# Kernel tuning notes

Measured on AMD Instinct MI355X. Metric: run time of the kernel, lower is better.

The kernel has to match this reference:

```python
import jax, jax.numpy as jnp
import numpy as np

NUM_HEADS = 16
HEAD_DIM = 64
ROPE_BASE = 160000.0


def _rope_tables(seq_len, head_dim):
    inv_freq = 1.0 / (ROPE_BASE ** (jnp.arange(0, head_dim, 2, dtype=jnp.float32) / head_dim))
    freqs = jnp.arange(seq_len, dtype=jnp.float32)[:, None] * inv_freq[None, :]  # [S, hd/2]
    return jnp.cos(freqs)[None, None], jnp.sin(freqs)[None, None]  # [1,1,S,hd/2]


def _apply_rope(x, cos, sin):
    # x: [B, nh, S, hd]; split-half rotation as in the torch module
    x1, x2 = jnp.split(x, 2, axis=-1)
    return jnp.concatenate([x1 * cos - x2 * sin, x2 * cos + x1 * sin], axis=-1)


def setup_inputs() -> dict:
    key = jax.random.key(0)
    k1, k2, k3 = jax.random.split(key, 3)
    B, S, H = 2, 2048, 1024
    hidden_states = jax.random.normal(k1, (B, S, H), dtype=jnp.float32)
    # additive causal mask: 0 for allowed, -1e9 for future positions
    causal = jnp.tril(jnp.ones((S, S), dtype=bool))
    attention_mask = jnp.where(causal, 0.0, -1e9).astype(jnp.float32)[None, None]
    Wqkv = jax.random.normal(k2, (H, 3 * H), dtype=jnp.float32) * (H ** -0.5)
    Wo = jax.random.normal(k3, (H, H), dtype=jnp.float32) * (H ** -0.5)
    return {"hidden_states": hidden_states, "attention_mask": attention_mask, "Wqkv": Wqkv, "Wo": Wo}


def reference(hidden_states, attention_mask, Wqkv, Wo):
    B, S, H = hidden_states.shape
    nh, hd = NUM_HEADS, HEAD_DIM
    scale = hd ** -0.5

    qkv = hidden_states @ Wqkv                                   # [B,S,3H]
    qkv = qkv.reshape(B, S, 3, nh, hd).transpose(2, 0, 3, 1, 4)  # [3,B,nh,S,hd]
    q, k, v = qkv[0], qkv[1], qkv[2]

    cos, sin = _rope_tables(S, hd)
    q = _apply_rope(q, cos, sin)
    k = _apply_rope(k, cos, sin)

    scores = jnp.einsum('bhqd,bhkd->bhqk', q, k) * scale + attention_mask
    attn = jax.nn.softmax(scores, axis=-1)
    out = jnp.einsum('bhqk,bhkd->bhqd', attn, v)                 # [B,nh,S,hd]
    out = out.transpose(0, 2, 1, 3).reshape(B, S, H)
    return out @ Wo
```

## Files before the change

kernel.cpp:

```cpp
#include <hip/hip_runtime.h>
#include <hip/hip_bf16.h>

typedef __bf16 bf16x8 __attribute__((ext_vector_type(8)));
typedef float f32x4 __attribute__((ext_vector_type(4)));
typedef unsigned short u16;

__device__ __forceinline__ u16 f2bf(float f) {
    union { float f; unsigned u; } x{f};
    unsigned r = x.u + 0x7fffu + ((x.u >> 16) & 1u);
    return (u16)(r >> 16);
}
__device__ __forceinline__ unsigned pk2(float a, float b) {
    union { float f; unsigned u; } x{a}, y{b};
    return ((x.u + 0x8000u) >> 16) | ((y.u + 0x8000u) & 0xffff0000u);
}
__device__ __forceinline__ float ex2(float x) { return __builtin_amdgcn_exp2f(x); }
__device__ __forceinline__ f32x4 zero4() { f32x4 z = {0.f, 0.f, 0.f, 0.f}; return z; }

typedef const __attribute__((address_space(1))) unsigned int* gp1_t;
typedef __attribute__((address_space(3))) unsigned int* lp3_t;
__device__ __forceinline__ void async16(const u16* g, u16* l) {
    __builtin_amdgcn_global_load_lds((gp1_t)g, (lp3_t)l, 16, 0, 0);
}

__global__ void __launch_bounds__(256) prep(const float* __restrict__ hs,
                                            u16* __restrict__ Xb,
                                            const float* __restrict__ Wqkv,
                                            u16* __restrict__ Wqkvt,
                                            const float* __restrict__ Wo,
                                            u16* __restrict__ Wot,
                                            float* __restrict__ cosT,
                                            float* __restrict__ sinT) {
    __shared__ float tile[32][33];
    const int blk = blockIdx.x, t = threadIdx.x;
    if (blk < 4096) {
        int i = (blk * 256 + t) * 4;
        float4 v = *(const float4*)(hs + i);
        ushort4 o;
        o.x = f2bf(v.x); o.y = f2bf(v.y); o.z = f2bf(v.z); o.w = f2bf(v.w);
        *(ushort4*)(Xb + i) = o;
    } else if (blk < 8192) {
        const float* W; u16* Wt; int N, bx, by;
        if (blk < 7168) { int bid = blk - 4096; W = Wqkv; Wt = Wqkvt; N = 3072; bx = bid % 96; by = bid / 96; }
        else            { int bid = blk - 7168; W = Wo;   Wt = Wot;   N = 1024; bx = bid % 32; by = bid / 32; }
        const int K = 1024;
        int tx = t & 31, ty = t >> 5;
        int n0 = bx * 32, k0 = by * 32;
#pragma unroll
        for (int i = 0; i < 32; i += 8)
            tile[ty + i][tx] = W[(size_t)(k0 + ty + i) * N + n0 + tx];
        __syncthreads();
#pragma unroll
        for (int i = 0; i < 32; i += 8)
            Wt[(size_t)(n0 + ty + i) * K + k0 + tx] = f2bf(tile[tx][ty + i]);
    } else {
        int idx = (blk - 8192) * 256 + t;
        int d = idx & 31, s = idx >> 5;
        float inv = expf(-(float)d * 0.374466538f);
        float th = (float)s * inv;
        cosT[idx] = cosf(th);
        sinT[idx] = sinf(th);
    }
}

struct GemmCtx {
    f32x4 acc[4][4];
    int m16, q4, wm, wn;
};
template <int KDIM>
__device__ __forceinline__ void gemm_loop(const u16* __restrict__ A,
                                          const u16* __restrict__ Bt,
                                          int bm, int bn, GemmCtx& cx,
                                          u16* As, u16* Bs) {
    const int t = threadIdx.x;
    const int lane = t & 63, w = t >> 6;
    cx.wm = w >> 1; cx.wn = w & 1;
    cx.m16 = lane & 15; cx.q4 = lane >> 4;

    const int lrow = lane >> 2;
    const int kchunk = (lane & 3) ^ ((lane >> 3) & 3);
    const u16* Ag = A + (size_t)(bm * 128 + w * 32 + lrow) * KDIM + kchunk * 8;
    const u16* Bg = Bt + (size_t)(bn * 128 + w * 32 + lrow) * KDIM + kchunk * 8;
    const int l0 = (w * 32) * 32;
    const int l1 = (w * 32 + 16) * 32;
    const int kswz = (cx.q4 ^ ((cx.m16 >> 1) & 3)) * 8;

#pragma unroll
    for (int i = 0; i < 4; i++)
#pragma unroll
        for (int j = 0; j < 4; j++) cx.acc[i][j] = zero4();

    constexpr int NT = KDIM / 32;
    async16(Ag, As + l0);
    async16(Ag + 16 * KDIM, As + l1);
    async16(Bg, Bs + l0);
    async16(Bg + 16 * KDIM, Bs + l1);

#pragma unroll 1
    for (int tt = 0; tt < NT; ++tt) {
        const int co = (tt & 1) * 4096;
        if (tt + 1 < NT) {
            const int no = 4096 - co;
            const int k0 = (tt + 1) * 32;
            async16(Ag + k0, As + no + l0);
            async16(Ag + 16 * KDIM + k0, As + no + l1);
            async16(Bg + k0, Bs + no + l0);
            async16(Bg + 16 * KDIM + k0, Bs + no + l1);
            asm volatile("s_waitcnt vmcnt(4)" ::: "memory");
        } else {
            asm volatile("s_waitcnt vmcnt(0)" ::: "memory");
        }
        __builtin_amdgcn_s_barrier();
        asm volatile("" ::: "memory");
        __builtin_amdgcn_sched_barrier(0);

        bf16x8 af[4], bf[4];
#pragma unroll
        for (int i = 0; i < 4; i++)
            af[i] = *(const bf16x8*)&As[co + (cx.wm * 64 + i * 16 + cx.m16) * 32 + kswz];
#pragma unroll
        for (int j = 0; j < 4; j++)
            bf[j] = *(const bf16x8*)&Bs[co + (cx.wn * 64 + j * 16 + cx.m16) * 32 + kswz];
#pragma unroll
        for (int i = 0; i < 4; i++)
#pragma unroll
            for (int j = 0; j < 4; j++)
                cx.acc[i][j] = __builtin_amdgcn_mfma_f32_16x16x32_bf16(af[i], bf[j], cx.acc[i][j], 0, 0, 0);

        asm volatile("" ::: "memory");
        __builtin_amdgcn_sched_barrier(0);
        __builtin_amdgcn_s_barrier();
    }
}

__global__ void __launch_bounds__(256) gemm_qkv(const u16* __restrict__ A,
                                                const u16* __restrict__ Bt,
                                                const float* __restrict__ cosT,
                                                const float* __restrict__ sinT,
                                                u16* __restrict__ Q,
                                                u16* __restrict__ Kd,
                                                u16* __restrict__ Vt) {
    __shared__ __align__(16) u16 As[2 * 128 * 32];
    __shared__ __align__(16) u16 Bs[2 * 128 * 32];
    GemmCtx cx;
    const int bm = blockIdx.y, bn = blockIdx.x;
    gemm_loop<1024>(A, Bt, bm, bn, cx, As, Bs);
    const int m16 = cx.m16, q4 = cx.q4;

    const int colbase = bn * 128 + cx.wn * 64;
    const int type = colbase >> 10;
    const int h = (colbase & 1023) >> 6;
    const int rbase = bm * 128 + cx.wm * 64;

    if (type == 2) {
#pragma unroll
        for (int i = 0; i < 4; i++) {
            int s0 = rbase + i * 16 + q4 * 4;
            int b = s0 >> 11, sl = s0 & 2047;
            size_t ob = (size_t)(b * 16 + h) * 64 * 2048;
#pragma unroll
            for (int j = 0; j < 4; j++) {
                int d = j * 16 + m16;
                ushort4 o;
                o.x = f2bf(cx.acc[i][j][0]);
                o.y = f2bf(cx.acc[i][j][1]);
                o.z = f2bf(cx.acc[i][j][2]);
                o.w = f2bf(cx.acc[i][j][3]);
                *(ushort4*)&Vt[ob + (size_t)d * 2048 + sl] = o;
            }
        }
    } else {
        u16* dst = (type == 0) ? Q : Kd;
        const float qs = (type == 0) ? 0.1803368801f  : 1.0f;
#pragma unroll
        for (int i = 0; i < 4; i++)
#pragma unroll
            for (int rr = 0; rr < 4; rr++) {
                int r = rbase + i * 16 + q4 * 4 + rr;
                int b = r >> 11, s = r & 2047;
                size_t ob = ((size_t)((b * 16 + h) * 2048 + s)) * 64;
#pragma unroll
                for (int j2 = 0; j2 < 2; j2++) {
                    int d = j2 * 16 + m16;
                    float cs = cosT[s * 32 + d];
                    float sn = sinT[s * 32 + d];
                    float x1 = cx.acc[i][j2][rr];
                    float x2 = cx.acc[i][j2 + 2][rr];
                    dst[ob + d]      = f2bf((x1 * cs - x2 * sn) * qs);
                    dst[ob + d + 32] = f2bf((x2 * cs + x1 * sn) * qs);
                }
            }
    }
}

__global__ void __launch_bounds__(256) gemm_out(const u16* __restrict__ A,
                                                const u16* __restrict__ Bt,
                                                float* __restrict__ C) {
    __shared__ __align__(16) u16 As[2 * 128 * 32];
    __shared__ __align__(16) u16 Bs[2 * 128 * 32];
    GemmCtx cx;
    const int bm = blockIdx.y, bn = blockIdx.x;
    gemm_loop<1024>(A, Bt, bm, bn, cx, As, Bs);
    const int N = 1024;
#pragma unroll
    for (int i = 0; i < 4; i++)
#pragma unroll
        for (int j = 0; j < 4; j++)
#pragma unroll
            for (int rr = 0; rr < 4; rr++) {
                int row = bm * 128 + cx.wm * 64 + i * 16 + cx.q4 * 4 + rr;
                int col = bn * 128 + cx.wn * 64 + j * 16 + cx.m16;
                C[(size_t)row * N + col] = cx.acc[i][j][rr];
            }
}

__global__ void __launch_bounds__(512) attn_kernel(const u16* __restrict__ Q,
                                                   const u16* __restrict__ Kg_,
                                                   const u16* __restrict__ Vtg_,
                                                   u16* __restrict__ O) {
    __shared__ __align__(16) u16 Ks[2][64][72];
    __shared__ __align__(16) u16 Vs[2][64][72];
    __shared__ __align__(16) u16 Pt[8][16][72];
    const int t = threadIdx.x, w = t >> 6;
    const int m16 = t & 15, q4 = (t & 63) >> 4;
    const int bx = blockIdx.x, bh = blockIdx.y;
    const size_t base = (size_t)bh * 2048 * 64;
    const int b = bh >> 4, h = bh & 15;
    const int skey = t >> 3, sc = (t & 7) * 8;

#pragma unroll 1
    for (int ph = 0; ph < 2; ph++) {
        const int st = ph ? (15 - bx) : bx;
        const int qrow = st * 128 + w * 16 + m16;
        const u16* Qg = Q + base + (size_t)qrow * 64;
        bf16x8 qf0 = *(const bf16x8*)(Qg + q4 * 8);
        bf16x8 qf1 = *(const bf16x8*)(Qg + 32 + q4 * 8);

        f32x4 occ[4];
#pragma unroll
        for (int dc = 0; dc < 4; dc++) occ[dc] = zero4();
        float li = 0.f;

        const int jtmax = 2 * st + 1;
        const int jd = 2 * st + (w >> 2);

        const u16* Kb0 = Kg_ + base + skey * 64 + sc;
        const u16* Vt0 = Vtg_ + base + (size_t)skey * 2048 + sc;
        uint4 ka = *(const uint4*)(Kb0);
        uint4 va = *(const uint4*)(Vt0);

#pragma unroll 1
        for (int jt = 0; jt <= jtmax; jt++) {
            const int bi = jt & 1;
            *(uint4*)&Ks[bi][skey][sc] = ka;
            *(uint4*)&Vs[bi][skey][sc] = va;
            if (jt < jtmax) {
                ka = *(const uint4*)(Kb0 + (size_t)(jt + 1) * 4096);
                va = *(const uint4*)(Vt0 + (size_t)(jt + 1) * 64);
            }
            __syncthreads();

            if (jt <= jd) {
                f32x4 stv[4];
#pragma unroll
                for (int c = 0; c < 4; c++) stv[c] = zero4();
#pragma unroll
                for (int c = 0; c < 4; c++) {
                    bf16x8 kf0 = *(const bf16x8*)&Ks[bi][c * 16 + m16][q4 * 8];
                    bf16x8 kf1 = *(const bf16x8*)&Ks[bi][c * 16 + m16][32 + q4 * 8];
                    stv[c] = __builtin_amdgcn_mfma_f32_16x16x32_bf16(kf0, qf0, stv[c], 0, 0, 0);
                    stv[c] = __builtin_amdgcn_mfma_f32_16x16x32_bf16(kf1, qf1, stv[c], 0, 0, 0);
                }

                float pv[4][4];
#pragma unroll
                for (int c = 0; c < 4; c++)
#pragma unroll
                    for (int rr = 0; rr < 4; rr++) pv[c][rr] = stv[c][rr];
                if (jt == jd) {
                    const int ql = qrow - 64 * jt;
#pragma unroll
                    for (int c = 0; c < 4; c++)
#pragma unroll
                        for (int rr = 0; rr < 4; rr++)
                            if (c * 16 + q4 * 4 + rr > ql) pv[c][rr] = -1e30f;
                }

#pragma unroll
                for (int c = 0; c < 4; c++) {
                    float p0 = ex2(pv[c][0] - 24.f);
                    float p1 = ex2(pv[c][1] - 24.f);
                    float p2 = ex2(pv[c][2] - 24.f);
                    float p3 = ex2(pv[c][3] - 24.f);
                    li += (p0 + p1) + (p2 + p3);
                    *(uint2*)&Pt[w][m16][c * 16 + q4 * 4] = make_uint2(pk2(p0, p1), pk2(p2, p3));
                }

#pragma unroll
                for (int ks = 0; ks < 2; ks++) {
                    bf16x8 pf = *(const bf16x8*)&Pt[w][m16][ks * 32 + q4 * 8];
#pragma unroll
                    for (int dc = 0; dc < 4; dc++) {
                        bf16x8 vf = *(const bf16x8*)&Vs[bi][dc * 16 + m16][ks * 32 + q4 * 8];
                        occ[dc] = __builtin_amdgcn_mfma_f32_16x16x32_bf16(vf, pf, occ[dc], 0, 0, 0);
                    }
                }
            }
        }

        li += __shfl_xor(li, 16);
        li += __shfl_xor(li, 32);
        float rli = 1.0f / li;
        u16* Op = O + ((size_t)(b * 2048 + qrow)) * 1024 + h * 64 + q4 * 4;
#pragma unroll
        for (int dc = 0; dc < 4; dc++) {
            ushort4 o;
            o.x = f2bf(occ[dc][0] * rli);
            o.y = f2bf(occ[dc][1] * rli);
            o.z = f2bf(occ[dc][2] * rli);
            o.w = f2bf(occ[dc][3] * rli);
            *(ushort4*)(Op + dc * 16) = o;
        }
        __syncthreads();
    }
}

extern "C" void kernel_launch(void* const* d_in, const int* in_sizes, int n_in,
                              void* d_out, int out_size, void* d_ws, size_t ws_size,
                              hipStream_t stream) {
    const float* hs   = (const float*)d_in[0];
    const float* Wqkv = (const float*)d_in[2];
    const float* Wo   = (const float*)d_in[3];
    float* out = (float*)d_out;

    const int BS = 4096;
    const int H = 1024, N3 = 3072;
    const int SH = 32 * 2048 * 64;

    u16* Xb    = (u16*)d_ws;
    u16* Wqkvt = Xb + (size_t)BS * H;
    u16* Wot   = Wqkvt + (size_t)N3 * H;
    u16* Qb    = Wot + (size_t)H * H;
    u16* Kb    = Qb + SH;
    u16* Vtb   = Kb + SH;
    u16* AOb   = Vtb + SH;
    float* cosT = (float*)(AOb + (size_t)BS * H);
    float* sinT = cosT + 2048 * 32;

    prep<<<8448, 256, 0, stream>>>(hs, Xb, Wqkv, Wqkvt, Wo, Wot, cosT, sinT);

    gemm_qkv<<<dim3(N3 / 128, BS / 128), 256, 0, stream>>>(Xb, Wqkvt, cosT, sinT,
                                                           Qb, Kb, Vtb);

    attn_kernel<<<dim3(8, 32), 512, 0, stream>>>(Qb, Kb, Vtb, AOb);

    gemm_out<<<dim3(H / 128, BS / 128), 256, 0, stream>>>(AOb, Wot, out);
}
```

Measured before the change: 200.9 us.

## Use 2-wave 64x128 warp tiles and XCD-aware block remap in QKV GEMM

Reworks the QKV projection GEMM to use 128 threads per block, with each of two waves computing a 64x128 sub-tile (4x8 MFMA accumulators). This raises operand reuse per LDS read and halves the waves per block. A 1D grid is remapped so consecutive blocks in each group of 8 land on the same chiplet, aiming for better L2 locality. The epilogue is extended to write two heads per wave. The larger accumulator footprint raises register pressure and may limit occupancy.

```diff
diff --git a/kernel.cpp b/kernel.cpp
--- a/kernel.cpp
+++ b/kernel.cpp
@@ -133,23 +133,96 @@
     }
 }
 
-__global__ void __launch_bounds__(256) gemm_qkv(const u16* __restrict__ A,
-                                                const u16* __restrict__ Bt,
-                                                const float* __restrict__ cosT,
-                                                const float* __restrict__ sinT,
-                                                u16* __restrict__ Q,
-                                                u16* __restrict__ Kd,
-                                                u16* __restrict__ Vt) {
+struct GemmCtx2 {
+    f32x4 acc[4][8];
+    int m16, q4, wm;
+};
+template <int KDIM>
+__device__ __forceinline__ void gemm_loop2(const u16* __restrict__ A,
+                                           const u16* __restrict__ Bt,
+                                           int bm, int bn, GemmCtx2& cx,
+                                           u16* As, u16* Bs) {
+    const int t = threadIdx.x;
+    const int lane = t & 63, w = t >> 6;
+    cx.wm = w;
+    cx.m16 = lane & 15; cx.q4 = lane >> 4;
+
+    const int lrow = lane >> 2;
+    const int kchunk = (lane & 3) ^ ((lane >> 3) & 3);
+    const u16* Ag = A + (size_t)(bm * 128 + w * 64 + lrow) * KDIM + kchunk * 8;
+    const u16* Bg = Bt + (size_t)(bn * 128 + w * 64 + lrow) * KDIM + kchunk * 8;
+    const int lb = (w * 64) * 32;
+    const int kswz = (cx.q4 ^ ((cx.m16 >> 1) & 3)) * 8;
+
+#pragma unroll
+    for (int i = 0; i < 4; i++)
+#pragma unroll
+        for (int j = 0; j < 8; j++) cx.acc[i][j] = zero4();
+
+    constexpr int NT = KDIM / 32;
+#pragma unroll
+    for (int c = 0; c < 4; c++) {
+        async16(Ag + c * 16 * KDIM, As + lb + c * 16 * 32);
+        async16(Bg + c * 16 * KDIM, Bs + lb + c * 16 * 32);
+    }
+
+#pragma unroll 1
+    for (int tt = 0; tt < NT; ++tt) {
+        const int co = (tt & 1) * 4096;
+        if (tt + 1 < NT) {
+            const int no = 4096 - co;
+            const int k0 = (tt + 1) * 32;
+#pragma unroll
+            for (int c = 0; c < 4; c++) {
+                async16(Ag + k0 + c * 16 * KDIM, As + no + lb + c * 16 * 32);
+                async16(Bg + k0 + c * 16 * KDIM, Bs + no + lb + c * 16 * 32);
+            }
+            asm volatile("s_waitcnt vmcnt(8)" ::: "memory");
+        } else {
+            asm volatile("s_waitcnt vmcnt(0)" ::: "memory");
+        }
+        __builtin_amdgcn_s_barrier();
+        asm volatile("" ::: "memory");
+        __builtin_amdgcn_sched_barrier(0);
+
+        bf16x8 af[4], bf[8];
+#pragma unroll
+        for (int i = 0; i < 4; i++)
+            af[i] = *(const bf16x8*)&As[co + (cx.wm * 64 + i * 16 + cx.m16) * 32 + kswz];
+#pragma unroll
+        for (int j = 0; j < 8; j++)
+            bf[j] = *(const bf16x8*)&Bs[co + (j * 16 + cx.m16) * 32 + kswz];
+#pragma unroll
+        for (int i = 0; i < 4; i++)
+#pragma unroll
+            for (int j = 0; j < 8; j++)
+                cx.acc[i][j] = __builtin_amdgcn_mfma_f32_16x16x32_bf16(af[i], bf[j], cx.acc[i][j], 0, 0, 0);
+
+        asm volatile("" ::: "memory");
+        __builtin_amdgcn_sched_barrier(0);
+        __builtin_amdgcn_s_barrier();
+    }
+}
+
+__global__ void __launch_bounds__(128, 2) gemm_qkv(const u16* __restrict__ A,
+                                                   const u16* __restrict__ Bt,
+                                                   const float* __restrict__ cosT,
+                                                   const float* __restrict__ sinT,
+                                                   u16* __restrict__ Q,
+                                                   u16* __restrict__ Kd,
+                                                   u16* __restrict__ Vt) {
     __shared__ __align__(16) u16 As[2 * 128 * 32];
     __shared__ __align__(16) u16 Bs[2 * 128 * 32];
-    GemmCtx cx;
-    const int bm = blockIdx.y, bn = blockIdx.x;
-    gemm_loop<1024>(A, Bt, bm, bn, cx, As, Bs);
+    GemmCtx2 cx;
+    const int hw = blockIdx.x;
+    const int orig = (hw & 7) * 96 + (hw >> 3);
+    const int bm = orig / 24, bn = orig % 24;
+    gemm_loop2<1024>(A, Bt, bm, bn, cx, As, Bs);
     const int m16 = cx.m16, q4 = cx.q4;
 
-    const int colbase = bn * 128 + cx.wn * 64;
-    const int type = colbase >> 10;
-    const int h = (colbase & 1023) >> 6;
+    const int colblk = bn * 128;
+    const int type = colblk >> 10;
+    const int h0 = (colblk & 1023) >> 6;
     const int rbase = bm * 128 + cx.wm * 64;
 
     if (type == 2) {
@@ -157,10 +230,11 @@
         for (int i = 0; i < 4; i++) {
             int s0 = rbase + i * 16 + q4 * 4;
             int b = s0 >> 11, sl = s0 & 2047;
-            size_t ob = (size_t)(b * 16 + h) * 64 * 2048;
-#pragma unroll
-            for (int j = 0; j < 4; j++) {
-                int d = j * 16 + m16;
+#pragma unroll
+            for (int j = 0; j < 8; j++) {
+                int h = h0 + (j >> 2);
+                int d = (j & 3) * 16 + m16;
+                size_t ob = (size_t)(b * 16 + h) * 64 * 2048;
                 ushort4 o;
                 o.x = f2bf(cx.acc[i][j][0]);
                 o.y = f2bf(cx.acc[i][j][1]);
@@ -178,16 +252,19 @@
             for (int rr = 0; rr < 4; rr++) {
                 int r = rbase + i * 16 + q4 * 4 + rr;
                 int b = r >> 11, s = r & 2047;
-                size_t ob = ((size_t)((b * 16 + h) * 2048 + s)) * 64;
-#pragma unroll
-                for (int j2 = 0; j2 < 2; j2++) {
-                    int d = j2 * 16 + m16;
-                    float cs = cosT[s * 32 + d];
-                    float sn = sinT[s * 32 + d];
-                    float x1 = cx.acc[i][j2][rr];
-                    float x2 = cx.acc[i][j2 + 2][rr];
-                    dst[ob + d]      = f2bf((x1 * cs - x2 * sn) * qs);
-                    dst[ob + d + 32] = f2bf((x2 * cs + x1 * sn) * qs);
+#pragma unroll
+                for (int hh = 0; hh < 2; hh++) {
+                    size_t ob = ((size_t)((b * 16 + h0 + hh) * 2048 + s)) * 64;
+#pragma unroll
+                    for (int j2 = 0; j2 < 2; j2++) {
+                        int d = j2 * 16 + m16;
+                        float cs = cosT[s * 32 + d];
+                        float sn = sinT[s * 32 + d];
+                        float x1 = cx.acc[i][hh * 4 + j2][rr];
+                        float x2 = cx.acc[i][hh * 4 + j2 + 2][rr];
+                        dst[ob + d]      = f2bf((x1 * cs - x2 * sn) * qs);
+                        dst[ob + d + 32] = f2bf((x2 * cs + x1 * sn) * qs);
+                    }
                 }
             }
     }
@@ -349,8 +426,7 @@
 
     prep<<<8448, 256, 0, stream>>>(hs, Xb, Wqkv, Wqkvt, Wo, Wot, cosT, sinT);
 
-    gemm_qkv<<<dim3(N3 / 128, BS / 128), 256, 0, stream>>>(Xb, Wqkvt, cosT, sinT,
-                                                           Qb, Kb, Vtb);
+    gemm_qkv<<<768, 128, 0, stream>>>(Xb, Wqkvt, cosT, sinT, Qb, Kb, Vtb);
 
     attn_kernel<<<dim3(8, 32), 512, 0, stream>>>(Qb, Kb, Vtb, AOb);
 
```

New measurement: 189.2 us. 5.8% less time.
